# Performance work log

Hardware: AMD Instinct MI355X
Metric: run time of the kernel (lower is better)

Reference implementation:

```python
import jax, jax.numpy as jnp
import numpy as np

# ---- dims ----
V, VR, E, H, NF = 100000, 5000, 300, 256, 150
H2 = 2 * H  # 512


def _lstm_dir(x, Wih, Whh, b, h0, c0):
    # x: (T, B, E); returns hs (T, B, H), final (h, c)
    def step(carry, xt):
        h, c = carry
        z = xt @ Wih.T + h @ Whh.T + b
        i, f, g, o = jnp.split(z, 4, axis=-1)  # torch gate order i,f,g,o
        c = jax.nn.sigmoid(f) * c + jax.nn.sigmoid(i) * jnp.tanh(g)
        h = jax.nn.sigmoid(o) * jnp.tanh(c)
        return (h, c), h
    (hT, cT), hs = jax.lax.scan(step, (h0, c0), x)
    return hs, hT, cT


def bilstm(x, Wih_f, Whh_f, b_f, Wih_b, Whh_b, b_b, state=None):
    # x: (T, B, E) -> out (T, B, 2H), state tuple
    B = x.shape[1]
    if state is None:
        z = jnp.zeros((B, H), x.dtype)
        state = (z, z, z, z)
    h0f, c0f, h0b, c0b = state
    hs_f, hTf, cTf = _lstm_dir(x, Wih_f, Whh_f, b_f, h0f, c0f)
    hs_b, hTb, cTb = _lstm_dir(x[::-1], Wih_b, Whh_b, b_b, h0b, c0b)
    out = jnp.concatenate([hs_f, hs_b[::-1]], axis=-1)
    return out, (hTf, cTf, hTb, cTb)


def abwim_atten(question_out, word_rel, rela_rel, word_emb, rela_emb,
                Wih_f, Whh_f, b_f, Wih_b, Whh_b, b_b, W):
    # question_out: (B, 2H, Sq); word_rel (B,Sw), rela_rel (B,Sr) int
    rela = rela_emb[rela_rel.T]   # (Sr, B, E)
    word = word_emb[word_rel.T]   # (Sw, B, E)
    word_out, state = bilstm(word, Wih_f, Whh_f, b_f, Wih_b, Whh_b, b_b)
    rela_out, _ = bilstm(rela, Wih_f, Whh_f, b_f, Wih_b, Whh_b, b_b, state)
    relation = jnp.concatenate([rela_out, word_out], axis=0).transpose(1, 0, 2)  # (B, R, 2H)
    energy = jnp.einsum('brh,hk,bks->brs', relation, W, question_out)  # (B, R, Sq)
    B, R, Sq = energy.shape
    scale = 1.0 / np.sqrt(R).astype(np.float32)
    alpha = jax.nn.softmax(energy.reshape(B, R * Sq) * scale, axis=-1).reshape(B, R, Sq)
    # sum_r alpha[b,r,s] * relation[b,r,h] -> (B, 2H, Sq)
    return jnp.einsum('brs,brh->bhs', alpha, relation)


def setup_inputs():
    key = jax.random.key(0)
    ks = jax.random.split(key, 24)
    B, Sq, Sw, Sr = 64, 40, 12, 4
    s_emb, s_lstm, s_w = 0.05, 0.05, 0.04
    inp = {
        'question': jax.random.randint(ks[0], (B, Sq), 0, V),
        'word_relation': jax.random.randint(ks[1], (B, Sw), 0, V),
        'rela_relation': jax.random.randint(ks[2], (B, Sr), 0, VR),
        'word_previous': jax.random.randint(ks[3], (B, Sw), 0, V),
        'rela_previous': jax.random.randint(ks[4], (B, Sr), 0, VR),
        'word_emb': jax.random.normal(ks[5], (V, E), jnp.float32) * s_emb,
        'rela_emb': jax.random.normal(ks[6], (VR, E), jnp.float32) * s_emb,
        'Wih_f': jax.random.normal(ks[7], (4 * H, E), jnp.float32) * s_lstm,
        'Whh_f': jax.random.normal(ks[8], (4 * H, H), jnp.float32) * s_lstm,
        'b_f': jnp.zeros((4 * H,), jnp.float32),
        'Wih_b': jax.random.normal(ks[9], (4 * H, E), jnp.float32) * s_lstm,
        'Whh_b': jax.random.normal(ks[10], (4 * H, H), jnp.float32) * s_lstm,
        'b_b': jnp.zeros((4 * H,), jnp.float32),
        'W': jax.random.normal(ks[11], (H2, H2), jnp.float32) * s_w,
        'cnn1_w': jax.random.normal(ks[12], (NF, 2 * H2, 1), jnp.float32) * s_w,
        'cnn1_b': jnp.zeros((NF,), jnp.float32),
        'cnn2_w': jax.random.normal(ks[13], (NF, 2 * H2, 3), jnp.float32) * s_w,
        'cnn2_b': jnp.zeros((NF,), jnp.float32),
        'cnn3_w': jax.random.normal(ks[14], (NF, 2 * H2, 5), jnp.float32) * s_w,
        'cnn3_b': jnp.zeros((NF,), jnp.float32),
        'lin_w': jax.random.normal(ks[15], (1, NF), jnp.float32) * s_w,
        'lin2_w': jax.random.normal(ks[16], (H2, H2), jnp.float32) * s_w,
        'lin2_b': jnp.zeros((H2,), jnp.float32),
    }
    return inp


def _conv1d(x, w, b):
    # x: (B, C, L), w: (O, C, K)
    y = jax.lax.conv_general_dilated(x, w, (1,), 'VALID',
                                     dimension_numbers=('NCH', 'OIH', 'NCH'))
    return y + b[None, :, None]


def reference(question, word_relation, rela_relation, word_previous, rela_previous,
              word_emb, rela_emb, Wih_f, Whh_f, b_f, Wih_b, Whh_b, b_b, W,
              cnn1_w, cnn1_b, cnn2_w, cnn2_b, cnn3_w, cnn3_b, lin_w, lin2_w, lin2_b):
    lstm_p = (Wih_f, Whh_f, b_f, Wih_b, Whh_b, b_b)
    # question encoder (dropout is identity at eval)
    q = word_emb[question.T]                      # (Sq, B, E)
    q_out, _ = bilstm(q, *lstm_p)                 # (Sq, B, 2H)
    question_out = q_out.transpose(1, 2, 0)       # (B, 2H, Sq)
    # reduce one previous hop
    atten_prev = abwim_atten(question_out, word_previous, rela_previous,
                             word_emb, rela_emb, *lstm_p, W)
    qo = question_out - atten_prev
    qo = qo.transpose(0, 2, 1) @ lin2_w.T + lin2_b   # (B, Sq, 2H)
    question_out = qo.transpose(0, 2, 1)             # (B, 2H, Sq)
    # current relation attention
    atten_relation = abwim_atten(question_out, word_relation, rela_relation,
                                 word_emb, rela_emb, *lstm_p, W)
    M = jnp.concatenate([question_out, atten_relation], axis=1)  # (B, 4H, Sq)
    h1 = jnp.max(jax.nn.relu(_conv1d(M, cnn1_w, cnn1_b)), axis=2)  # (B, NF)
    h2 = jnp.max(jax.nn.relu(_conv1d(M, cnn2_w, cnn2_b)), axis=2)
    h3 = jnp.max(jax.nn.relu(_conv1d(M, cnn3_w, cnn3_b)), axis=2)
    h = jnp.maximum(jnp.maximum(h1, h2), h3)
    score = (h @ lin_w.T).squeeze(-1)  # (B,)
    return score
```

## Files before the change

kernel.cpp:

```cpp
#include <hip/hip_runtime.h>
#include <math.h>

#define NEG_INF (-3.402823466e+38f)

typedef __attribute__((ext_vector_type(8))) short short8;
typedef __attribute__((ext_vector_type(8))) unsigned short ushort8;
typedef __attribute__((ext_vector_type(4))) float f32x4;

constexpr int NTOK = 4608;
constexpr int BH = 64 * 256;

constexpr size_t OFF_WQ    = 0;
constexpr size_t OFF_B2    = OFF_WQ    + 524288;
constexpr size_t OFF_XB3T  = OFF_B2    + 2048;
constexpr size_t OFF_WB3T  = OFF_XB3T  + 983040;
constexpr size_t OFF_L2B3T = OFF_WB3T  + 393216;
constexpr size_t OFF_C1B3T = OFF_L2B3T + 393216;
constexpr size_t OFF_C2B3T = OFF_C1B3T + 294912;
constexpr size_t OFF_C3B3T = OFF_C2B3T + 884736;
constexpr size_t OFF_XHI   = OFF_C3B3T + 1474560;
constexpr size_t OFF_XLO   = OFF_XHI   + 737280;
constexpr size_t OFF_XP    = OFF_XLO   + 737280;
constexpr size_t OFF_HSQ   = OFF_XP    + 9437184;
constexpr size_t OFF_HSWP  = OFF_HSQ   + 1310720;
constexpr size_t OFF_HSRP  = OFF_HSWP  + 393216;
constexpr size_t OFF_HSWR  = OFF_HSRP  + 131072;
constexpr size_t OFF_HSRR  = OFF_HSWR  + 393216;
constexpr size_t OFF_CS    = OFF_HSRR  + 131072;
constexpr size_t OFF_RELP  = OFF_CS    + 163840;
constexpr size_t OFF_RELC  = OFF_RELP  + 524288;
constexpr size_t OFF_RELW  = OFF_RELC  + 524288;
constexpr size_t OFF_EN    = OFF_RELW  + 524288;

__device__ inline unsigned short f2bf(float f) {
  unsigned int u = __float_as_uint(f);
  u += 0x7FFFu + ((u >> 16) & 1u);
  return (unsigned short)(u >> 16);
}
__device__ inline float bf2f(unsigned short h) {
  return __uint_as_float(((unsigned int)h) << 16);
}

__global__ __launch_bounds__(256) void k_prep(
    const float* __restrict__ Whh_f, const float* __restrict__ Whh_b,
    const float* __restrict__ b_f,   const float* __restrict__ b_b,
    const float* __restrict__ Wih_f, const float* __restrict__ Wih_b,
    const float* __restrict__ Wat,   const float* __restrict__ l2w,
    const float* __restrict__ c1w, const float* __restrict__ c2w, const float* __restrict__ c3w,
    unsigned short* __restrict__ WHB, float* __restrict__ B2,
    unsigned short* __restrict__ XB3T, unsigned short* __restrict__ WB3T,
    unsigned short* __restrict__ L2B3T,
    unsigned short* __restrict__ C1B3T, unsigned short* __restrict__ C2B3T,
    unsigned short* __restrict__ C3B3T, int* __restrict__ bar) {
  if (blockIdx.x == 0 && threadIdx.x < 8)
    __hip_atomic_store(bar + threadIdx.x, 0, __ATOMIC_RELAXED, __HIP_MEMORY_SCOPE_AGENT);
  int idx = blockIdx.x * 256 + threadIdx.x;
  if (idx < 1048576) {
    int e = idx & 511;
    int k = e & 255, isLo = e >> 8;
    int row = (idx >> 9) & 63;
    int tile = (idx >> 15) & 15;
    int d = idx >> 19;
    int g = row >> 4, uu = row & 15;
    int u = tile * 16 + uu;
    const float* Wh = d ? Whh_b : Whh_f;
    float w = Wh[(size_t)(g * 256 + u) * 256 + k];
    unsigned short hi = f2bf(w);
    WHB[idx] = isLo ? f2bf(w - bf2f(hi)) : hi;
    return;
  }
  idx -= 1048576;
  if (idx < 2048) { B2[idx] = (idx < 1024) ? b_f[idx] : b_b[idx-1024]; return; }
  idx -= 2048;
  unsigned short* dst; int n, k, K;
  float w;
  if (idx < 655360) {
    n = idx / 320; k = idx % 320; K = 320; dst = XB3T;
    w = (k < 300) ? ((n < 1024) ? Wih_f[(size_t)n*300 + k] : Wih_b[(size_t)(n-1024)*300 + k]) : 0.f;
  } else if ((idx -= 655360) < 262144) {
    n = idx >> 9; k = idx & 511; K = 512; dst = WB3T;
    w = Wat[(size_t)k*512 + n];
  } else if ((idx -= 262144) < 262144) {
    n = idx >> 9; k = idx & 511; K = 512; dst = L2B3T;
    w = l2w[(size_t)n*512 + k];
  } else if ((idx -= 262144) < 196608) {
    n = idx >> 10; k = idx & 1023; K = 1024; dst = C1B3T;
    w = (n < 150) ? c1w[(size_t)n*1024 + k] : 0.f;
  } else if ((idx -= 196608) < 589824) {
    n = idx / 3072; k = idx % 3072; K = 3072; dst = C2B3T;
    int kw = k >> 10, c = k & 1023;
    w = (n < 150) ? c2w[((size_t)n*1024 + c)*3 + kw] : 0.f;
  } else if ((idx -= 589824) < 983040) {
    n = idx / 5120; k = idx % 5120; K = 5120; dst = C3B3T;
    int kw = k >> 10, c = k & 1023;
    w = (n < 150) ? c3w[((size_t)n*1024 + c)*5 + kw] : 0.f;
  } else return;
  unsigned short hi = f2bf(w);
  unsigned short lo = f2bf(w - bf2f(hi));
  size_t base = (size_t)n * (3*K);
  dst[base + k] = hi;
  dst[base + K + k] = lo;
  dst[base + 2*K + k] = hi;
}

__global__ __launch_bounds__(320) void k_gather(
    const int* __restrict__ q,  const int* __restrict__ wr, const int* __restrict__ rr,
    const int* __restrict__ wp, const int* __restrict__ rp,
    const float* __restrict__ we, const float* __restrict__ re,
    unsigned short* __restrict__ Xhi, unsigned short* __restrict__ Xlo) {
  int m = blockIdx.x, k = threadIdx.x;
  const float* emb; int row;
  if (m < 2560)      { int t=m>>6,    b=m&63; row = q [b*40+t]; emb = we; }
  else if (m < 3328) { int mm=m-2560; int t=mm>>6,b=mm&63; row = wp[b*12+t]; emb = we; }
  else if (m < 3584) { int mm=m-3328; int t=mm>>6,b=mm&63; row = rp[b*4 +t]; emb = re; }
  else if (m < 4352) { int mm=m-3584; int t=mm>>6,b=mm&63; row = wr[b*12+t]; emb = we; }
  else               { int mm=m-4352; int t=mm>>6,b=mm&63; row = rr[b*4 +t]; emb = re; }
  float v = (k < 300) ? emb[(size_t)row*300 + k] : 0.f;
  unsigned short hi = f2bf(v);
  Xhi[(size_t)m*320 + k] = hi;
  Xlo[(size_t)m*320 + k] = f2bf(v - bf2f(hi));
}

template<bool BIAS>
__global__ __launch_bounds__(256) void k_mgemm(
    const unsigned short* __restrict__ Ahi, const unsigned short* __restrict__ Alo, int lda,
    const unsigned short* __restrict__ Bt, const float* __restrict__ bias,
    float* __restrict__ C, int N, int K) {
  __shared__ unsigned short As[64 * 40];
  __shared__ unsigned short Bs[64 * 40];
  int tid = threadIdx.x;
  int wave = tid >> 6, lane = tid & 63;
  int quad = lane >> 4, l16 = lane & 15;
  int m0 = blockIdx.x << 6, n0 = blockIdx.y << 6;
  int K3 = 3 * K;
  int sr = tid >> 2;
  int sc = (tid & 3) << 3;
  f32x4 acc[4] = {};
  for (int k0 = 0; k0 < K3; k0 += 32) {
    int c = (k0 >= K) + (k0 >= 2*K);
    const unsigned short* Asrc = (c == 2) ? Alo : Ahi;
    int kk = k0 - c * K;
    ushort8 av = *(const ushort8*)(Asrc + (size_t)(m0 + sr) * lda + kk + sc);
    ushort8 bv = *(const ushort8*)(Bt + (size_t)(n0 + sr) * K3 + k0 + sc);
    *(ushort8*)&As[sr * 40 + sc] = av;
    *(ushort8*)&Bs[sr * 40 + sc] = bv;
    __syncthreads();
    short8 a  = *(const short8*)&As[(wave*16 + l16) * 40 + quad*8];
    short8 b0 = *(const short8*)&Bs[( 0 + l16) * 40 + quad*8];
    short8 b1 = *(const short8*)&Bs[(16 + l16) * 40 + quad*8];
    short8 b2 = *(const short8*)&Bs[(32 + l16) * 40 + quad*8];
    short8 b3 = *(const short8*)&Bs[(48 + l16) * 40 + quad*8];
    acc[0] = __builtin_amdgcn_mfma_f32_16x16x32_bf16(a, b0, acc[0], 0, 0, 0);
    acc[1] = __builtin_amdgcn_mfma_f32_16x16x32_bf16(a, b1, acc[1], 0, 0, 0);
    acc[2] = __builtin_amdgcn_mfma_f32_16x16x32_bf16(a, b2, acc[2], 0, 0, 0);
    acc[3] = __builtin_amdgcn_mfma_f32_16x16x32_bf16(a, b3, acc[3], 0, 0, 0);
    __syncthreads();
  }
  int row0 = m0 + wave * 16 + quad * 4;
#pragma unroll
  for (int t = 0; t < 4; t++) {
    int col = n0 + t * 16 + l16;
    float bb = BIAS ? bias[col] : 0.f;
#pragma unroll
    for (int r = 0; r < 4; r++)
      C[(size_t)(row0 + r) * N + col] = acc[t][r] + bb;
  }
}

__global__ __launch_bounds__(256) void k_cgemm(
    const unsigned short* __restrict__ Ahi, const unsigned short* __restrict__ Alo,
    const unsigned short* __restrict__ B1, const unsigned short* __restrict__ B2c,
    const unsigned short* __restrict__ B3,
    float* __restrict__ Y1, float* __restrict__ Y2, float* __restrict__ Y3) {
  __shared__ unsigned short As[64 * 40];
  __shared__ unsigned short Bs[64 * 40];
  int z = blockIdx.z;
  const unsigned short* Bt; float* Y; int K, sidx, chunk;
  if (z < 4)       { Bt = B1;  Y = Y1; K = 1024; sidx = z;      chunk = 768;  }
  else if (z < 12) { Bt = B2c; Y = Y2; K = 3072; sidx = z - 4;  chunk = 1152; }
  else             { Bt = B3;  Y = Y3; K = 5120; sidx = z - 12; chunk = 1920; }
  int K3 = 3 * K;
  int ks = sidx * chunk, ke = ks + chunk;
  int tid = threadIdx.x;
  int wave = tid >> 6, lane = tid & 63;
  int quad = lane >> 4, l16 = lane & 15;
  int m0 = blockIdx.x << 6, n0 = blockIdx.y << 6;
  int sr = tid >> 2;
  int sc = (tid & 3) << 3;
  f32x4 acc[4] = {};
  for (int k0 = ks; k0 < ke; k0 += 32) {
    int c = (k0 >= K) + (k0 >= 2*K);
    const unsigned short* Asrc = (c == 2) ? Alo : Ahi;
    int kk = k0 - c * K;
    ushort8 av = *(const ushort8*)(Asrc + (size_t)(m0 + sr) * 1024 + kk + sc);
    ushort8 bv = *(const ushort8*)(Bt + (size_t)(n0 + sr) * K3 + k0 + sc);
    *(ushort8*)&As[sr * 40 + sc] = av;
    *(ushort8*)&Bs[sr * 40 + sc] = bv;
    __syncthreads();
    short8 a  = *(const short8*)&As[(wave*16 + l16) * 40 + quad*8];
    short8 b0 = *(const short8*)&Bs[( 0 + l16) * 40 + quad*8];
    short8 b1 = *(const short8*)&Bs[(16 + l16) * 40 + quad*8];
    short8 b2 = *(const short8*)&Bs[(32 + l16) * 40 + quad*8];
    short8 b3 = *(const short8*)&Bs[(48 + l16) * 40 + quad*8];
    acc[0] = __builtin_amdgcn_mfma_f32_16x16x32_bf16(a, b0, acc[0], 0, 0, 0);
    acc[1] = __builtin_amdgcn_mfma_f32_16x16x32_bf16(a, b1, acc[1], 0, 0, 0);
    acc[2] = __builtin_amdgcn_mfma_f32_16x16x32_bf16(a, b2, acc[2], 0, 0, 0);
    acc[3] = __builtin_amdgcn_mfma_f32_16x16x32_bf16(a, b3, acc[3], 0, 0, 0);
    __syncthreads();
  }
  int row0 = m0 + wave * 16 + quad * 4;
#pragma unroll
  for (int t = 0; t < 4; t++) {
    int col = n0 + t * 16 + l16;
#pragma unroll
    for (int r = 0; r < 4; r++)
      atomicAdd(&Y[(size_t)(row0 + r) * 192 + col], acc[t][r]);
  }
}

__global__ __launch_bounds__(256) void k_zero(float* __restrict__ p, int n4) {
  int idx = blockIdx.x * 256 + threadIdx.x;
  if (idx < n4) *(float4*)(p + (size_t)idx * 4) = make_float4(0.f, 0.f, 0.f, 0.f);
}

__global__ __launch_bounds__(256) void k_steps(
    const unsigned short* __restrict__ WHB, const float* __restrict__ XP,
    float* __restrict__ hsQ, float* __restrict__ hsWp, float* __restrict__ hsRp,
    float* __restrict__ hsWr, float* __restrict__ hsRr,
    unsigned int* __restrict__ Hx, int* __restrict__ bar) {
  constexpr int S = 520;
  __shared__ unsigned short Ws[64 * S];
  __shared__ unsigned short Hs[64 * S];
  int bid = blockIdx.x;
  int chain = bid & 7;
  if (chain >= 6) return;
  int tile = bid >> 3;
  int dir = chain & 1, fam = chain >> 1;
  int tid = threadIdx.x;
  int wave = tid >> 6, lane = tid & 63;
  int quad = lane >> 4, l16 = lane & 15;
  int u0 = tile << 4;

  const unsigned short* wsrc = WHB + (((size_t)dir * 16 + tile) << 15);
#pragma unroll
  for (int j = 0; j < 16; j++) {
    int i = j * 256 + tid;
    *(ushort8*)&Ws[(i >> 6) * S + (i & 63) * 8] = *(const ushort8*)(wsrc + i * 8);
  }
  __syncthreads();

  int nsteps = (fam == 0) ? 40 : 16;
  float creg[4] = {0.f, 0.f, 0.f, 0.f};
  int arow = (wave * 16 + l16) * S + quad * 8;
  int brow = l16 * S + quad * 8;

  for (int cs = 0; cs < nsteps; cs++) {
    f32x4 acc[4] = {};
    if (cs > 0) {
      if (tid == 0) {
        int tgt = 16 * cs;
        while (__hip_atomic_load(bar + chain, __ATOMIC_RELAXED, __HIP_MEMORY_SCOPE_AGENT) < tgt)
          __builtin_amdgcn_s_sleep(2);
      }
      __syncthreads();
      unsigned long long* hp =
          (unsigned long long*)(Hx + (((size_t)(chain * 2 + ((cs - 1) & 1))) << 14));
#pragma unroll
      for (int jj = 0; jj < 2; jj++) {
        unsigned long long vbuf[16];
#pragma unroll
        for (int j2 = 0; j2 < 16; j2++)
          vbuf[j2] = __hip_atomic_load(hp + (jj * 16 + j2) * 256 + tid,
                                       __ATOMIC_RELAXED, __HIP_MEMORY_SCOPE_AGENT);
#pragma unroll
        for (int j2 = 0; j2 < 16; j2++) {
          int w = (jj * 16 + j2) * 256 + tid;
          int b = w >> 7, u = (w & 127) * 2;
          unsigned int w0 = (unsigned int)vbuf[j2], w1 = (unsigned int)(vbuf[j2] >> 32);
          *(unsigned int*)&Hs[b * S + u]       = (w0 & 0xFFFFu) | (w1 << 16);
          *(unsigned int*)&Hs[b * S + 256 + u] = (w0 >> 16) | (w1 & 0xFFFF0000u);
        }
      }
      __syncthreads();
#pragma unroll
      for (int c = 0; c < 3; c++) {
        int ao = (c == 2) ? 256 : 0, bo = (c == 1) ? 256 : 0;
#pragma unroll
        for (int ks = 0; ks < 256; ks += 32) {
          short8 a = *(const short8*)&Hs[arow + ao + ks];
#pragma unroll
          for (int nf = 0; nf < 4; nf++) {
            short8 bf = *(const short8*)&Ws[brow + nf * 16 * S + bo + ks];
            acc[nf] = __builtin_amdgcn_mfma_f32_16x16x32_bf16(a, bf, acc[nf], 0, 0, 0);
          }
        }
      }
      __syncthreads();
    }
    int t, T, seg; float* hsb;
    if (fam == 0)     { t = cs;      T = 40; seg = 0;                         hsb = hsQ + (size_t)dir * 40 * BH; }
    else if (cs < 12) { t = cs;      T = 12; seg = (fam == 1) ? 2560 : 3584;  hsb = ((fam == 1) ? hsWp : hsWr) + (size_t)dir * 12 * BH; }
    else              { t = cs - 12; T = 4;  seg = (fam == 1) ? 3328 : 4352;  hsb = ((fam == 1) ? hsRp : hsRr) + (size_t)dir * 4 * BH; }
    int t_in = dir ? (T - 1 - t) : t;
    int u = u0 + l16;
    const float* xb = XP + (size_t)(seg + t_in * 64) * 2048 + dir * 1024 + u;
    float* hout = hsb + (size_t)t * BH + u;
    unsigned int* op = Hx + (((size_t)(chain * 2 + (cs & 1))) << 14) + u;
#pragma unroll
    for (int r = 0; r < 4; r++) {
      int b = wave * 16 + quad * 4 + r;
      const float* xr = xb + (size_t)b * 2048;
      float zi = acc[0][r] + xr[0];
      float zf = acc[1][r] + xr[256];
      float zg = acc[2][r] + xr[512];
      float zo = acc[3][r] + xr[768];
      float gi = 1.f / (1.f + expf(-zi));
      float gf = 1.f / (1.f + expf(-zf));
      float go = 1.f / (1.f + expf(-zo));
      float gg = tanhf(zg);
      float cn = gf * creg[r] + gi * gg;
      float hn = go * tanhf(cn);
      creg[r] = cn;
      hout[(size_t)b * 256] = hn;
      unsigned short hi = f2bf(hn);
      unsigned short lo = f2bf(hn - bf2f(hi));
      __hip_atomic_store(op + b * 256, (unsigned int)hi | ((unsigned int)lo << 16),
                         __ATOMIC_RELAXED, __HIP_MEMORY_SCOPE_AGENT);
    }
    if (cs + 1 < nsteps) {
      __syncthreads();
      if (tid == 0)
        __hip_atomic_fetch_add(bar + chain, 1, __ATOMIC_RELAXED, __HIP_MEMORY_SCOPE_AGENT);
    }
  }
}

__global__ __launch_bounds__(256) void k_qo1(const float* __restrict__ hsQ, float* __restrict__ QT) {
  int idx = blockIdx.x * 256 + threadIdx.x;
  if (idx >= 64*40*512) return;
  int h = idx & 511; int t2 = idx >> 9; int s = t2 % 40; int b = t2 / 40;
  float v;
  if (h < 256) v = hsQ[(size_t)s * BH + b*256 + h];
  else         v = hsQ[(size_t)40 * BH + (size_t)(39 - s) * BH + b*256 + (h - 256)];
  QT[idx] = v;
}

__global__ __launch_bounds__(256) void k_rel(
    const float* __restrict__ hsWp, const float* __restrict__ hsRp,
    const float* __restrict__ hsWr, const float* __restrict__ hsRr,
    float* __restrict__ RELP, float* __restrict__ RELC,
    unsigned short* __restrict__ RPhi, unsigned short* __restrict__ RPlo,
    unsigned short* __restrict__ RChi, unsigned short* __restrict__ RClo) {
  int idx0 = blockIdx.x * 256 + threadIdx.x;
  if (idx0 >= 2*64*16*512) return;
  int call = idx0 >= 64*16*512;
  int idx = idx0 - call * 64*16*512;
  int h = idx & 511; int t2 = idx >> 9; int r = t2 & 15; int b = t2 >> 4;
  const float* hsW = call ? hsWr : hsWp;
  const float* hsR = call ? hsRr : hsRp;
  float v;
  if (r < 4) {
    if (h < 256) v = hsR[(size_t)r * BH + b*256 + h];
    else         v = hsR[(size_t)4 * BH + (size_t)(3 - r) * BH + b*256 + (h - 256)];
  } else {
    int t = r - 4;
    if (h < 256) v = hsW[(size_t)t * BH + b*256 + h];
    else         v = hsW[(size_t)12 * BH + (size_t)(11 - t) * BH + b*256 + (h - 256)];
  }
  unsigned short hi = f2bf(v);
  unsigned short lo = f2bf(v - bf2f(hi));
  if (call) { RELC[idx] = v; RChi[idx] = hi; RClo[idx] = lo; }
  else      { RELP[idx] = v; RPhi[idx] = hi; RPlo[idx] = lo; }
}

__global__ __launch_bounds__(256) void k_energy(
    const float* __restrict__ relW, const float* __restrict__ QT, float* __restrict__ EN) {
  int idx = blockIdx.x * 256 + threadIdx.x;
  if (idx >= 64*16*40) return;
  int s = idx % 40; int t = idx / 40; int r = t & 15; int b = t >> 4;
  const float* rw = relW + (size_t)(b*16 + r) * 512;
  const float* qv = QT   + (size_t)(b*40 + s) * 512;
  float acc = 0.f;
#pragma unroll 4
  for (int k = 0; k < 512; k += 4) {
    float4 a = *(const float4*)(rw + k);
    float4 c = *(const float4*)(qv + k);
    acc += a.x*c.x + a.y*c.y + a.z*c.z + a.w*c.w;
  }
  EN[idx] = acc;
}

__global__ __launch_bounds__(256) void k_softmax(float* __restrict__ EN) {
  int b = blockIdx.x; int tid = threadIdx.x;
  float* e = EN + b * 640;
  float v0 = e[tid] * 0.25f, v1 = e[tid + 256] * 0.25f;
  float v2 = (tid < 128) ? e[tid + 512] * 0.25f : NEG_INF;
  __shared__ float sh[256];
  sh[tid] = fmaxf(v0, fmaxf(v1, v2));
  __syncthreads();
  for (int st = 128; st > 0; st >>= 1) { if (tid < st) sh[tid] = fmaxf(sh[tid], sh[tid+st]); __syncthreads(); }
  float m = sh[0];
  __syncthreads();
  float e0 = expf(v0 - m), e1 = expf(v1 - m);
  float e2 = (tid < 128) ? expf(v2 - m) : 0.f;
  sh[tid] = e0 + e1 + e2;
  __syncthreads();
  for (int st = 128; st > 0; st >>= 1) { if (tid < st) sh[tid] += sh[tid+st]; __syncthreads(); }
  float inv = 1.f / sh[0];
  e[tid] = e0 * inv; e[tid + 256] = e1 * inv;
  if (tid < 128) e[tid + 512] = e2 * inv;
}

__global__ __launch_bounds__(256) void k_atten(
    const float* __restrict__ AL, const float* __restrict__ REL, float* __restrict__ ATT) {
  int idx = blockIdx.x * 256 + threadIdx.x;
  if (idx >= 64*40*512) return;
  int h = idx & 511; int t2 = idx >> 9; int s = t2 % 40; int b = t2 / 40;
  const float* al = AL + b * 640 + s;
  const float* rl = REL + (size_t)b * 16 * 512 + h;
  float acc = 0.f;
#pragma unroll
  for (int r = 0; r < 16; r++) acc += al[r*40] * rl[r*512];
  ATT[idx] = acc;
}

__global__ __launch_bounds__(256) void k_sub(
    const float* __restrict__ QT, const float* __restrict__ ATT,
    unsigned short* __restrict__ Dhi, unsigned short* __restrict__ Dlo) {
  int idx = blockIdx.x * 256 + threadIdx.x;
  if (idx >= 64*40*512) return;
  float v = QT[idx] - ATT[idx];
  unsigned short hi = f2bf(v);
  Dhi[idx] = hi; Dlo[idx] = f2bf(v - bf2f(hi));
}

__global__ __launch_bounds__(256) void k_m2(
    const float* __restrict__ QO2, const float* __restrict__ ATT,
    unsigned short* __restrict__ M2hi, unsigned short* __restrict__ M2lo) {
  int idx = blockIdx.x * 256 + threadIdx.x;
  if (idx >= 2626048) return;
  float v = 0.f;
  if (idx < 2621440) {
    int c = idx & 1023; int m = idx >> 10;
    v = (c < 512) ? QO2[(size_t)m*512 + c] : ATT[(size_t)m*512 + (c - 512)];
  }
  unsigned short hi = f2bf(v);
  M2hi[idx] = hi; M2lo[idx] = f2bf(v - bf2f(hi));
}

__global__ __launch_bounds__(256) void k_pool(
    const float* __restrict__ Y1, const float* __restrict__ Y2, const float* __restrict__ Y3,
    const float* __restrict__ b1, const float* __restrict__ b2, const float* __restrict__ b3,
    const float* __restrict__ lw, float* __restrict__ out) {
  int b = blockIdx.x, o = threadIdx.x;
  float hv = 0.f;
  if (o < 150) {
    const float* y1 = Y1 + (size_t)b*40*192 + o;
    const float* y2 = Y2 + (size_t)b*40*192 + o;
    const float* y3 = Y3 + (size_t)b*40*192 + o;
    float m1 = NEG_INF, m2 = NEG_INF, m3 = NEG_INF;
#pragma unroll 4
    for (int l = 0; l < 40; l++) m1 = fmaxf(m1, y1[l*192]);
#pragma unroll 2
    for (int l = 0; l < 38; l++) m2 = fmaxf(m2, y2[l*192]);
#pragma unroll 2
    for (int l = 0; l < 36; l++) m3 = fmaxf(m3, y3[l*192]);
    float h = fmaxf(fmaxf(m1 + b1[o], m2 + b2[o]), m3 + b3[o]);
    hv = fmaxf(h, 0.f) * lw[o];
  }
  __shared__ float sh[256];
  sh[threadIdx.x] = hv;
  __syncthreads();
  for (int st = 128; st > 0; st >>= 1) { if (threadIdx.x < st) sh[threadIdx.x] += sh[threadIdx.x+st]; __syncthreads(); }
  if (threadIdx.x == 0) out[b] = sh[0];
}

extern "C" void kernel_launch(void* const* d_in, const int* in_sizes, int n_in,
                              void* d_out, int out_size, void* d_ws, size_t ws_size,
                              hipStream_t stream) {
  const int*   q    = (const int*)d_in[0];
  const int*   wrel = (const int*)d_in[1];
  const int*   rrel = (const int*)d_in[2];
  const int*   wprv = (const int*)d_in[3];
  const int*   rprv = (const int*)d_in[4];
  const float* we   = (const float*)d_in[5];
  const float* re   = (const float*)d_in[6];
  const float* Wih_f= (const float*)d_in[7];
  const float* Whh_f= (const float*)d_in[8];
  const float* b_f  = (const float*)d_in[9];
  const float* Wih_b= (const float*)d_in[10];
  const float* Whh_b= (const float*)d_in[11];
  const float* b_b  = (const float*)d_in[12];
  const float* W    = (const float*)d_in[13];
  const float* c1w  = (const float*)d_in[14];
  const float* c1b  = (const float*)d_in[15];
  const float* c2w  = (const float*)d_in[16];
  const float* c2b  = (const float*)d_in[17];
  const float* c3w  = (const float*)d_in[18];
  const float* c3b  = (const float*)d_in[19];
  const float* lw   = (const float*)d_in[20];
  const float* l2w  = (const float*)d_in[21];
  const float* l2b  = (const float*)d_in[22];
  float* out = (float*)d_out;
  float* ws  = (float*)d_ws;

  unsigned short* WHB = (unsigned short*)(ws + OFF_WQ);
  float* B2   = ws + OFF_B2;
  unsigned short* XB3T  = (unsigned short*)(ws + OFF_XB3T);
  unsigned short* WB3T  = (unsigned short*)(ws + OFF_WB3T);
  unsigned short* L2B3T = (unsigned short*)(ws + OFF_L2B3T);
  unsigned short* C1B3T = (unsigned short*)(ws + OFF_C1B3T);
  unsigned short* C2B3T = (unsigned short*)(ws + OFF_C2B3T);
  unsigned short* C3B3T = (unsigned short*)(ws + OFF_C3B3T);
  unsigned short* Xhi   = (unsigned short*)(ws + OFF_XHI);
  unsigned short* Xlo   = (unsigned short*)(ws + OFF_XLO);
  float* XP   = ws + OFF_XP;
  float* HSQ  = ws + OFF_HSQ;
  float* HSWP = ws + OFF_HSWP;
  float* HSRP = ws + OFF_HSRP;
  float* HSWR = ws + OFF_HSWR;
  float* HSRR = ws + OFF_HSRR;
  int*   bar  = (int*)(ws + OFF_CS);
  float* RELP = ws + OFF_RELP;
  float* RELC = ws + OFF_RELC;
  float* RELW = ws + OFF_RELW;
  float* EN   = ws + OFF_EN;
  unsigned int* Hx = (unsigned int*)(ws + OFF_RELP);
  float* QO1  = XP;
  float* ATT  = XP + 1310720;
  float* QO2  = XP + 2621440;
  unsigned short* Dhi  = (unsigned short*)(XP + 3932160);
  unsigned short* Dlo  = (unsigned short*)(XP + 4587520);
  unsigned short* RPhi = (unsigned short*)(XP + 5242880);
  unsigned short* RPlo = (unsigned short*)(XP + 5505024);
  unsigned short* RChi = (unsigned short*)(XP + 5767168);
  unsigned short* RClo = (unsigned short*)(XP + 6029312);
  unsigned short* M2hi = (unsigned short*)(XP + 5242880);
  unsigned short* M2lo = (unsigned short*)(XP + 6555904);
  float* Y1   = XP + 7868928;
  float* Y2   = XP + 8360448;
  float* Y3   = XP + 8851968;

  k_prep<<<15624, 256, 0, stream>>>(Whh_f, Whh_b, b_f, b_b, Wih_f, Wih_b, W, l2w,
                                    c1w, c2w, c3w,
                                    WHB, B2, XB3T, WB3T, L2B3T, C1B3T, C2B3T, C3B3T, bar);
  k_gather<<<NTOK, 320, 0, stream>>>(q, wrel, rrel, wprv, rprv, we, re, Xhi, Xlo);
  { dim3 g(72, 32); k_mgemm<true><<<g, 256, 0, stream>>>(Xhi, Xlo, 320, XB3T, B2, XP, 2048, 320); }

  k_steps<<<128, 256, 0, stream>>>(WHB, XP, HSQ, HSWP, HSRP, HSWR, HSRR, Hx, bar);

  k_qo1<<<5120, 256, 0, stream>>>(HSQ, QO1);
  k_rel<<<4096, 256, 0, stream>>>(HSWP, HSRP, HSWR, HSRR, RELP, RELC, RPhi, RPlo, RChi, RClo);

  { dim3 g(16, 8); k_mgemm<false><<<g, 256, 0, stream>>>(RPhi, RPlo, 512, WB3T, nullptr, RELW, 512, 512); }
  k_energy<<<160, 256, 0, stream>>>(RELW, QO1, EN);
  k_softmax<<<64, 256, 0, stream>>>(EN);
  k_atten<<<5120, 256, 0, stream>>>(EN, RELP, ATT);
  k_sub<<<5120, 256, 0, stream>>>(QO1, ATT, Dhi, Dlo);
  { dim3 g(40, 8); k_mgemm<true><<<g, 256, 0, stream>>>(Dhi, Dlo, 512, L2B3T, l2b, QO2, 512, 512); }

  { dim3 g(16, 8); k_mgemm<false><<<g, 256, 0, stream>>>(RChi, RClo, 512, WB3T, nullptr, RELW, 512, 512); }
  k_energy<<<160, 256, 0, stream>>>(RELW, QO2, EN);
  k_softmax<<<64, 256, 0, stream>>>(EN);
  k_atten<<<5120, 256, 0, stream>>>(EN, RELC, ATT);

  k_m2<<<10258, 256, 0, stream>>>(QO2, ATT, M2hi, M2lo);
  k_zero<<<1440, 256, 0, stream>>>(Y1, 368640);
  { dim3 g(40, 3, 20); k_cgemm<<<g, 256, 0, stream>>>(M2hi, M2lo, C1B3T, C2B3T, C3B3T, Y1, Y2, Y3); }
  k_pool<<<64, 256, 0, stream>>>(Y1, Y2, Y3, c1b, c2b, c3b, lw, out);
}
```

Measured before the change: 776.4 us.

## Keep recurrent LSTM weights in registers and read hidden state directly from global

```diff
diff --git a/kernel.cpp b/kernel.cpp
--- a/kernel.cpp
+++ b/kernel.cpp
@@ -40,6 +40,11 @@
 __device__ inline float bf2f(unsigned short h) {
   return __uint_as_float(((unsigned int)h) << 16);
 }
+__device__ inline short8 mk8(unsigned long long a, unsigned long long b) {
+  union { unsigned long long q[2]; short8 s; } u;
+  u.q[0] = a; u.q[1] = b; return u.s;
+}
+#define ALD(p) __hip_atomic_load((p), __ATOMIC_RELAXED, __HIP_MEMORY_SCOPE_AGENT)
 
 __global__ __launch_bounds__(256) void k_prep(
     const float* __restrict__ Whh_f, const float* __restrict__ Whh_b,
@@ -223,14 +228,12 @@
   if (idx < n4) *(float4*)(p + (size_t)idx * 4) = make_float4(0.f, 0.f, 0.f, 0.f);
 }
 
-__global__ __launch_bounds__(256) void k_steps(
+__global__ __launch_bounds__(256, 1) void k_steps(
     const unsigned short* __restrict__ WHB, const float* __restrict__ XP,
     float* __restrict__ hsQ, float* __restrict__ hsWp, float* __restrict__ hsRp,
     float* __restrict__ hsWr, float* __restrict__ hsRr,
-    unsigned int* __restrict__ Hx, int* __restrict__ bar) {
-  constexpr int S = 520;
-  __shared__ unsigned short Ws[64 * S];
-  __shared__ unsigned short Hs[64 * S];
+    unsigned short* __restrict__ Hhi, unsigned short* __restrict__ Hlo,
+    int* __restrict__ bar) {
   int bid = blockIdx.x;
   int chain = bid & 7;
   if (chain >= 6) return;
@@ -242,61 +245,21 @@
   int u0 = tile << 4;
 
   const unsigned short* wsrc = WHB + (((size_t)dir * 16 + tile) << 15);
-#pragma unroll
-  for (int j = 0; j < 16; j++) {
-    int i = j * 256 + tid;
-    *(ushort8*)&Ws[(i >> 6) * S + (i & 63) * 8] = *(const ushort8*)(wsrc + i * 8);
-  }
-  __syncthreads();
+  short8 Bh[4][8], Bl[4][8];
+#pragma unroll
+  for (int nf = 0; nf < 4; nf++)
+#pragma unroll
+    for (int j = 0; j < 8; j++) {
+      const unsigned short* wr = wsrc + (nf * 16 + l16) * 512 + j * 32 + quad * 8;
+      Bh[nf][j] = *(const short8*)(wr);
+      Bl[nf][j] = *(const short8*)(wr + 256);
+    }
 
   int nsteps = (fam == 0) ? 40 : 16;
   float creg[4] = {0.f, 0.f, 0.f, 0.f};
-  int arow = (wave * 16 + l16) * S + quad * 8;
-  int brow = l16 * S + quad * 8;
+  int row64 = (wave * 16 + l16) * 64 + quad * 2;
 
   for (int cs = 0; cs < nsteps; cs++) {
-    f32x4 acc[4] = {};
-    if (cs > 0) {
-      if (tid == 0) {
-        int tgt = 16 * cs;
-        while (__hip_atomic_load(bar + chain, __ATOMIC_RELAXED, __HIP_MEMORY_SCOPE_AGENT) < tgt)
-          __builtin_amdgcn_s_sleep(2);
-      }
-      __syncthreads();
-      unsigned long long* hp =
-          (unsigned long long*)(Hx + (((size_t)(chain * 2 + ((cs - 1) & 1))) << 14));
-#pragma unroll
-      for (int jj = 0; jj < 2; jj++) {
-        unsigned long long vbuf[16];
-#pragma unroll
-        for (int j2 = 0; j2 < 16; j2++)
-          vbuf[j2] = __hip_atomic_load(hp + (jj * 16 + j2) * 256 + tid,
-                                       __ATOMIC_RELAXED, __HIP_MEMORY_SCOPE_AGENT);
-#pragma unroll
-        for (int j2 = 0; j2 < 16; j2++) {
-          int w = (jj * 16 + j2) * 256 + tid;
-          int b = w >> 7, u = (w & 127) * 2;
-          unsigned int w0 = (unsigned int)vbuf[j2], w1 = (unsigned int)(vbuf[j2] >> 32);
-          *(unsigned int*)&Hs[b * S + u]       = (w0 & 0xFFFFu) | (w1 << 16);
-          *(unsigned int*)&Hs[b * S + 256 + u] = (w0 >> 16) | (w1 & 0xFFFF0000u);
-        }
-      }
-      __syncthreads();
-#pragma unroll
-      for (int c = 0; c < 3; c++) {
-        int ao = (c == 2) ? 256 : 0, bo = (c == 1) ? 256 : 0;
-#pragma unroll
-        for (int ks = 0; ks < 256; ks += 32) {
-          short8 a = *(const short8*)&Hs[arow + ao + ks];
-#pragma unroll
-          for (int nf = 0; nf < 4; nf++) {
-            short8 bf = *(const short8*)&Ws[brow + nf * 16 * S + bo + ks];
-            acc[nf] = __builtin_amdgcn_mfma_f32_16x16x32_bf16(a, bf, acc[nf], 0, 0, 0);
-          }
-        }
-      }
-      __syncthreads();
-    }
     int t, T, seg; float* hsb;
     if (fam == 0)     { t = cs;      T = 40; seg = 0;                         hsb = hsQ + (size_t)dir * 40 * BH; }
     else if (cs < 12) { t = cs;      T = 12; seg = (fam == 1) ? 2560 : 3584;  hsb = ((fam == 1) ? hsWp : hsWr) + (size_t)dir * 12 * BH; }
@@ -304,16 +267,65 @@
     int t_in = dir ? (T - 1 - t) : t;
     int u = u0 + l16;
     const float* xb = XP + (size_t)(seg + t_in * 64) * 2048 + dir * 1024 + u;
+    float xi[4], xf[4], xg[4], xo[4];
+#pragma unroll
+    for (int r = 0; r < 4; r++) {
+      const float* xr = xb + (size_t)(wave * 16 + quad * 4 + r) * 2048;
+      xi[r] = xr[0]; xf[r] = xr[256]; xg[r] = xr[512]; xo[r] = xr[768];
+    }
+
+    f32x4 acc[4] = {};
+    if (cs > 0) {
+      if (tid == 0) {
+        int tgt = 16 * cs;
+        while (__hip_atomic_load(bar + chain, __ATOMIC_RELAXED, __HIP_MEMORY_SCOPE_AGENT) < tgt)
+          __builtin_amdgcn_s_sleep(1);
+      }
+      __syncthreads();
+      size_t slotq = (size_t)(chain * 2 + ((cs - 1) & 1)) * 4096;
+      const unsigned long long* ph = (const unsigned long long*)Hhi + slotq + row64;
+      const unsigned long long* pl = (const unsigned long long*)Hlo + slotq + row64;
+      unsigned long long rv[32];
+#pragma unroll
+      for (int j = 0; j < 8; j++) { rv[2*j] = ALD(ph + 8*j); rv[2*j+1] = ALD(ph + 8*j + 1); }
+#pragma unroll
+      for (int j = 0; j < 8; j++) { rv[16+2*j] = ALD(pl + 8*j); rv[16+2*j+1] = ALD(pl + 8*j + 1); }
+      short8 ah[8], al[8];
+#pragma unroll
+      for (int j = 0; j < 8; j++) { ah[j] = mk8(rv[2*j], rv[2*j+1]); al[j] = mk8(rv[16+2*j], rv[16+2*j+1]); }
+#pragma unroll
+      for (int j = 0; j < 8; j++) {
+        acc[0] = __builtin_amdgcn_mfma_f32_16x16x32_bf16(ah[j], Bh[0][j], acc[0], 0, 0, 0);
+        acc[1] = __builtin_amdgcn_mfma_f32_16x16x32_bf16(ah[j], Bh[1][j], acc[1], 0, 0, 0);
+        acc[2] = __builtin_amdgcn_mfma_f32_16x16x32_bf16(ah[j], Bh[2][j], acc[2], 0, 0, 0);
+        acc[3] = __builtin_amdgcn_mfma_f32_16x16x32_bf16(ah[j], Bh[3][j], acc[3], 0, 0, 0);
+      }
+#pragma unroll
+      for (int j = 0; j < 8; j++) {
+        acc[0] = __builtin_amdgcn_mfma_f32_16x16x32_bf16(ah[j], Bl[0][j], acc[0], 0, 0, 0);
+        acc[1] = __builtin_amdgcn_mfma_f32_16x16x32_bf16(ah[j], Bl[1][j], acc[1], 0, 0, 0);
+        acc[2] = __builtin_amdgcn_mfma_f32_16x16x32_bf16(ah[j], Bl[2][j], acc[2], 0, 0, 0);
+        acc[3] = __builtin_amdgcn_mfma_f32_16x16x32_bf16(ah[j], Bl[3][j], acc[3], 0, 0, 0);
+      }
+#pragma unroll
+      for (int j = 0; j < 8; j++) {
+        acc[0] = __builtin_amdgcn_mfma_f32_16x16x32_bf16(al[j], Bh[0][j], acc[0], 0, 0, 0);
+        acc[1] = __builtin_amdgcn_mfma_f32_16x16x32_bf16(al[j], Bh[1][j], acc[1], 0, 0, 0);
+        acc[2] = __builtin_amdgcn_mfma_f32_16x16x32_bf16(al[j], Bh[2][j], acc[2], 0, 0, 0);
+        acc[3] = __builtin_amdgcn_mfma_f32_16x16x32_bf16(al[j], Bh[3][j], acc[3], 0, 0, 0);
+      }
+    }
     float* hout = hsb + (size_t)t * BH + u;
-    unsigned int* op = Hx + (((size_t)(chain * 2 + (cs & 1))) << 14) + u;
+    size_t oslot = (size_t)(chain * 2 + (cs & 1)) << 14;
+    unsigned short* oh = Hhi + oslot;
+    unsigned short* ol = Hlo + oslot;
 #pragma unroll
     for (int r = 0; r < 4; r++) {
       int b = wave * 16 + quad * 4 + r;
-      const float* xr = xb + (size_t)b * 2048;
-      float zi = acc[0][r] + xr[0];
-      float zf = acc[1][r] + xr[256];
-      float zg = acc[2][r] + xr[512];
-      float zo = acc[3][r] + xr[768];
+      float zi = acc[0][r] + xi[r];
+      float zf = acc[1][r] + xf[r];
+      float zg = acc[2][r] + xg[r];
+      float zo = acc[3][r] + xo[r];
       float gi = 1.f / (1.f + expf(-zi));
       float gf = 1.f / (1.f + expf(-zf));
       float go = 1.f / (1.f + expf(-zo));
@@ -321,11 +333,19 @@
       float cn = gf * creg[r] + gi * gg;
       float hn = go * tanhf(cn);
       creg[r] = cn;
+      unsigned short h16 = f2bf(hn);
+      unsigned short l16v = f2bf(hn - bf2f(h16));
+      unsigned int pk = (unsigned int)h16 | ((unsigned int)l16v << 16);
+      unsigned int pw = (unsigned int)__shfl_xor((int)pk, 1, 64);
+      if ((lane & 1) == 0) {
+        unsigned int hw = (pk & 0xFFFFu) | (pw << 16);
+        unsigned int lw = (pk >> 16) | (pw & 0xFFFF0000u);
+        __hip_atomic_store((unsigned int*)(oh + b * 256 + u), hw,
+                           __ATOMIC_RELAXED, __HIP_MEMORY_SCOPE_AGENT);
+        __hip_atomic_store((unsigned int*)(ol + b * 256 + u), lw,
+                           __ATOMIC_RELAXED, __HIP_MEMORY_SCOPE_AGENT);
+      }
       hout[(size_t)b * 256] = hn;
-      unsigned short hi = f2bf(hn);
-      unsigned short lo = f2bf(hn - bf2f(hi));
-      __hip_atomic_store(op + b * 256, (unsigned int)hi | ((unsigned int)lo << 16),
-                         __ATOMIC_RELAXED, __HIP_MEMORY_SCOPE_AGENT);
     }
     if (cs + 1 < nsteps) {
       __syncthreads();
@@ -525,7 +545,8 @@
   float* RELC = ws + OFF_RELC;
   float* RELW = ws + OFF_RELW;
   float* EN   = ws + OFF_EN;
-  unsigned int* Hx = (unsigned int*)(ws + OFF_RELP);
+  unsigned short* Hhi = (unsigned short*)(ws + OFF_RELP);
+  unsigned short* Hlo = Hhi + 196608;
   float* QO1  = XP;
   float* ATT  = XP + 1310720;
   float* QO2  = XP + 2621440;
@@ -547,7 +568,7 @@
   k_gather<<<NTOK, 320, 0, stream>>>(q, wrel, rrel, wprv, rprv, we, re, Xhi, Xlo);
   { dim3 g(72, 32); k_mgemm<true><<<g, 256, 0, stream>>>(Xhi, Xlo, 320, XB3T, B2, XP, 2048, 320); }
 
-  k_steps<<<128, 256, 0, stream>>>(WHB, XP, HSQ, HSWP, HSRP, HSWR, HSRR, Hx, bar);
+  k_steps<<<128, 256, 0, stream>>>(WHB, XP, HSQ, HSWP, HSRP, HSWR, HSRR, Hhi, Hlo, bar);
 
   k_qo1<<<5120, 256, 0, stream>>>(HSQ, QO1);
   k_rel<<<4096, 256, 0, stream>>>(HSWP, HSRP, HSWR, HSRR, RELP, RELC, RPhi, RPlo, RChi, RClo);
```

After: 789.8 us. No clear change (+1.7%).
